# Performance work log

Hardware: AMD Instinct MI355X
Metric: run time of the kernel (lower is better)

## Reference

```python
import jax, jax.numpy as jnp
import numpy as np

H = 64
EPS = 1e-5


def _lstm_layer(x, w_ih, w_hh, b_ih, b_hh):
    """Single LSTM layer, batch_first input x: [B, T, I]. PyTorch gate order i,f,g,o."""
    B, T, _ = x.shape
    # precompute input contributions for all timesteps: [B, T, 4H]
    xw = jnp.einsum('bti,gi->btg', x, w_ih) + (b_ih + b_hh)
    xw = jnp.swapaxes(xw, 0, 1)  # [T, B, 4H] for scan over time

    def step(carry, xw_t):
        h, c = carry
        gates = xw_t + h @ w_hh.T  # [B, 4H]
        i, f, g, o = jnp.split(gates, 4, axis=-1)
        i = jax.nn.sigmoid(i)
        f = jax.nn.sigmoid(f)
        g = jnp.tanh(g)
        o = jax.nn.sigmoid(o)
        c = f * c + i * g
        h = o * jnp.tanh(c)
        return (h, c), h

    h0 = jnp.zeros((B, H), x.dtype)
    (_, _), hs = jax.lax.scan(step, (h0, h0), xw)
    return jnp.swapaxes(hs, 0, 1)  # [B, T, H]


def setup_inputs() -> dict:
    key = jax.random.key(0)
    ks = jax.random.split(key, 16)
    B, T, F = 4096, 256, 32
    s = 1.0 / np.sqrt(H)  # PyTorch LSTM init scale
    inp = {
        'x': jax.random.normal(ks[0], (B, T, F), jnp.float32),
        'w_ih0': jax.random.uniform(ks[1], (4 * H, F), jnp.float32, -s, s),
        'w_hh0': jax.random.uniform(ks[2], (4 * H, H), jnp.float32, -s, s),
        'b_ih0': jax.random.uniform(ks[3], (4 * H,), jnp.float32, -s, s),
        'b_hh0': jax.random.uniform(ks[4], (4 * H,), jnp.float32, -s, s),
        'w_ih1': jax.random.uniform(ks[5], (4 * H, H), jnp.float32, -s, s),
        'w_hh1': jax.random.uniform(ks[6], (4 * H, H), jnp.float32, -s, s),
        'b_ih1': jax.random.uniform(ks[7], (4 * H,), jnp.float32, -s, s),
        'b_hh1': jax.random.uniform(ks[8], (4 * H,), jnp.float32, -s, s),
        'ln_g': jnp.ones((H,), jnp.float32),
        'ln_b': jnp.zeros((H,), jnp.float32),
        'w1': jax.random.uniform(ks[9], (64, H), jnp.float32, -s, s),
        'b1': jax.random.uniform(ks[10], (64,), jnp.float32, -s, s),
        'w2': jax.random.uniform(ks[11], (1, 64), jnp.float32, -0.125, 0.125),
        'b2': jax.random.uniform(ks[12], (1,), jnp.float32, -0.125, 0.125),
    }
    return inp


def reference(x, w_ih0, w_hh0, b_ih0, b_hh0, w_ih1, w_hh1, b_ih1, b_hh1,
              ln_g, ln_b, w1, b1, w2, b2):
    out0 = _lstm_layer(x, w_ih0, w_hh0, b_ih0, b_hh0)      # [B, T, H]
    out1 = _lstm_layer(out0, w_ih1, w_hh1, b_ih1, b_hh1)   # [B, T, H]
    last = out1[:, -1, :]                                   # [B, H]
    # LayerNorm
    mu = jnp.mean(last, axis=-1, keepdims=True)
    var = jnp.mean(jnp.square(last - mu), axis=-1, keepdims=True)
    ln = (last - mu) * jax.lax.rsqrt(var + EPS) * ln_g + ln_b
    # MLP head
    h = jax.nn.relu(ln @ w1.T + b1)
    y = h @ w2.T + b2                                       # [B, 1]
    return y[:, 0]
```

## Files before the change

kernel.cpp:

```cpp
#include <hip/hip_runtime.h>

#define TSEQ 256
#define FIN  32
#define HID  64

typedef _Float16 f16x8 __attribute__((ext_vector_type(8)));
typedef float    f32x4 __attribute__((ext_vector_type(4)));

__device__ __forceinline__ float wsum(float v) {
    #pragma unroll
    for (int off = 32; off > 0; off >>= 1) v += __shfl_xor(v, off, 64);
    return v;
}

__device__ __forceinline__ float lstm_cell(const f32x4 g, float& c) {
    float ei = __expf(-g[0]);
    float ef = __expf(-g[1]);
    float yg = __expf(2.0f * g[2]);
    float eo = __expf(-g[3]);
    float sf = __builtin_amdgcn_rcpf(1.0f + ef);
    float ig = (yg - 1.0f) * __builtin_amdgcn_rcpf((1.0f + ei) * (yg + 1.0f));
    c = fmaf(sf, c, ig);
    float cc = fminf(fmaxf(c, -15.0f), 15.0f);
    float yc = __expf(2.0f * cc);
    return (yc - 1.0f) * __builtin_amdgcn_rcpf((1.0f + eo) * (yc + 1.0f));
}

__global__ __launch_bounds__(1024, 4)
void lstm_fused(const float* __restrict__ x,
                const float* __restrict__ w_ih0, const float* __restrict__ w_hh0,
                const float* __restrict__ b_ih0, const float* __restrict__ b_hh0,
                const float* __restrict__ w_ih1, const float* __restrict__ w_hh1,
                const float* __restrict__ b_ih1, const float* __restrict__ b_hh1,
                const float* __restrict__ ln_g, const float* __restrict__ ln_b,
                const float* __restrict__ w1, const float* __restrict__ b1,
                const float* __restrict__ w2, const float* __restrict__ b2,
                float* __restrict__ out)
{
    __shared__ __align__(16) _Float16 X[2][16][32];
    __shared__ __align__(16) _Float16 H0[2][16][72];
    __shared__ __align__(16) _Float16 H1[2][16][72];
    __shared__ __align__(16) float HF[16][68];
    __shared__ __align__(16) float LNB[16][64];

    const int tid  = threadIdx.x;
    const int wave = tid >> 6;
    const int lane = tid & 63;
    const int q    = lane >> 4;
    const int lm   = lane & 15;
    const int q8   = q * 8;
    const int b0   = blockIdx.x * 16;

    const int np   = wave * 16 + lm;
    const int drow = np >> 2;
    const int ty   = np & 3;
    const int row  = ty * 64 + drow;
    const int dq   = wave * 4 + q;

    f16x8 w0f[3], w1f[4];
    f32x4 bias0, bias1;
    {
        const float* p0 = w_ih0 + row * FIN + q8;
        const float* p1 = w_hh0 + row * HID + q8;
        const float* p2 = w_hh0 + row * HID + 32 + q8;
        const float* p3 = w_ih1 + row * HID + q8;
        const float* p4 = w_ih1 + row * HID + 32 + q8;
        const float* p5 = w_hh1 + row * HID + q8;
        const float* p6 = w_hh1 + row * HID + 32 + q8;
        #pragma unroll
        for (int j = 0; j < 8; ++j) {
            w0f[0][j] = (_Float16)p0[j];
            w0f[1][j] = (_Float16)p1[j];
            w0f[2][j] = (_Float16)p2[j];
            w1f[0][j] = (_Float16)p3[j];
            w1f[1][j] = (_Float16)p4[j];
            w1f[2][j] = (_Float16)p5[j];
            w1f[3][j] = (_Float16)p6[j];
        }
        #pragma unroll
        for (int r = 0; r < 4; ++r) {
            bias0[r] = b_ih0[r * 64 + dq] + b_hh0[r * 64 + dq];
            bias1[r] = b_ih1[r * 64 + dq] + b_hh1[r * 64 + dq];
        }
    }

    for (int i = tid; i < 2 * 16 * 72; i += 1024) {
        ((_Float16*)H0)[i] = (_Float16)0.0f;
        ((_Float16*)H1)[i] = (_Float16)0.0f;
    }
    const bool xlane = lane < 32;
    const int  xcol  = lane & 31;
    const float* xbase = x + (size_t)(b0 + wave) * TSEQ * FIN + xcol;
    if (xlane) X[0][wave][xcol] = (_Float16)xbase[0];
    float xw = xbase[FIN];

    float c0 = 0.0f, c1 = 0.0f;
    __syncthreads();

#define INTERVAL(P, DO_A, DO_B, DO_XSTORE, DO_XLOAD, XI)                        \
    {                                                                           \
        float xnew = 0.0f;                                                      \
        if (DO_XLOAD) xnew = xbase[(size_t)(XI) * FIN];                         \
        f16x8 rh0a = *reinterpret_cast<const f16x8*>(&H0[(P) ^ 1][lm][q8]);     \
        f16x8 rh0b = *reinterpret_cast<const f16x8*>(&H0[(P) ^ 1][lm][32 + q8]);\
        if (DO_A) {                                                             \
            f16x8 rx = *reinterpret_cast<const f16x8*>(&X[P][lm][q8]);          \
            f32x4 aA = bias0;                                                   \
            aA = __builtin_amdgcn_mfma_f32_16x16x32_f16(w0f[0], rx,   aA, 0, 0, 0); \
            aA = __builtin_amdgcn_mfma_f32_16x16x32_f16(w0f[1], rh0a, aA, 0, 0, 0); \
            aA = __builtin_amdgcn_mfma_f32_16x16x32_f16(w0f[2], rh0b, aA, 0, 0, 0); \
            float hA = lstm_cell(aA, c0);                                       \
            H0[P][lm][dq] = (_Float16)hA;                                       \
        }                                                                       \
        if (DO_B) {                                                             \
            f16x8 rh1a = *reinterpret_cast<const f16x8*>(&H1[P][lm][q8]);       \
            f16x8 rh1b = *reinterpret_cast<const f16x8*>(&H1[P][lm][32 + q8]);  \
            f32x4 aB = bias1;                                                   \
            aB = __builtin_amdgcn_mfma_f32_16x16x32_f16(w1f[0], rh0a, aB, 0, 0, 0); \
            aB = __builtin_amdgcn_mfma_f32_16x16x32_f16(w1f[1], rh0b, aB, 0, 0, 0); \
            aB = __builtin_amdgcn_mfma_f32_16x16x32_f16(w1f[2], rh1a, aB, 0, 0, 0); \
            aB = __builtin_amdgcn_mfma_f32_16x16x32_f16(w1f[3], rh1b, aB, 0, 0, 0); \
            float hB = lstm_cell(aB, c1);                                       \
            H1[(P) ^ 1][lm][dq] = (_Float16)hB;                                 \
            lastB = hB;                                                         \
        }                                                                       \
        if (DO_XSTORE && xlane) X[(P) ^ 1][wave][xcol] = (_Float16)xw;          \
        xw = xnew;                                                              \
        __syncthreads();                                                        \
    }

    float lastB = 0.0f;

    INTERVAL(0, true, false, true, true, 2)

    #pragma unroll 1
    for (int ii = 0; ii < 127; ++ii) {
        const int i1  = 2 * ii + 1;
        const int xiA = (i1 + 2 > 255) ? 255 : i1 + 2;
        const int xiB = (i1 + 3 > 255) ? 255 : i1 + 3;
        INTERVAL(1, true, true, true, true, xiA)
        INTERVAL(0, true, true, true, true, xiB)
    }

    INTERVAL(1, true, true, false, false, 0)
    INTERVAL(0, false, true, false, false, 0)
    HF[lm][dq] = lastB;
    __syncthreads();

#undef INTERVAL

    const float lngv = ln_g[lane], lnbv = ln_b[lane];
    const float b1v = b1[lane], w2v = w2[lane];
    const float* w1row = w1 + lane * 64;
    {
        float v  = HF[wave][lane];
        float mu = wsum(v) * (1.0f / 64.0f);
        float dv = v - mu;
        float var = wsum(dv * dv) * (1.0f / 64.0f);
        float ln = dv * rsqrtf(var + 1e-5f) * lngv + lnbv;
        LNB[wave][lane] = ln;
        float s = b1v;
        #pragma unroll
        for (int dd = 0; dd < 64; ++dd)
            s = fmaf(LNB[wave][dd], w1row[dd], s);
        s = fmaxf(s, 0.0f);
        float y = wsum(s * w2v);
        if (lane == 0) out[b0 + wave] = y + b2[0];
    }
}

extern "C" void kernel_launch(void* const* d_in, const int* in_sizes, int n_in,
                              void* d_out, int out_size, void* d_ws, size_t ws_size,
                              hipStream_t stream) {
    const float* x     = (const float*)d_in[0];
    const float* w_ih0 = (const float*)d_in[1];
    const float* w_hh0 = (const float*)d_in[2];
    const float* b_ih0 = (const float*)d_in[3];
    const float* b_hh0 = (const float*)d_in[4];
    const float* w_ih1 = (const float*)d_in[5];
    const float* w_hh1 = (const float*)d_in[6];
    const float* b_ih1 = (const float*)d_in[7];
    const float* b_hh1 = (const float*)d_in[8];
    const float* ln_g  = (const float*)d_in[9];
    const float* ln_b  = (const float*)d_in[10];
    const float* w1    = (const float*)d_in[11];
    const float* b1    = (const float*)d_in[12];
    const float* w2    = (const float*)d_in[13];
    const float* b2    = (const float*)d_in[14];
    lstm_fused<<<dim3(256), dim3(1024), 0, stream>>>(
        x, w_ih0, w_hh0, b_ih0, b_hh0,
        w_ih1, w_hh1, b_ih1, b_hh1,
        ln_g, ln_b, w1, b1, w2, b2, (float*)d_out);
}
```

Measured before the change: 370.5 us.

## Halve batch per block and split gate tiles across two MFMA sets per wave

Each block now handles 8 sequences with 8 waves instead of 16 sequences with 16 waves. Each wave keeps two gate-tile weight sets and issues two interleaved MFMA chains per layer. The 16-column MFMA is half-used, with the upper 8 columns padded by zeroed X. The two accumulators are merged into one lane-packed f32x4 via a DPP row-rotate, so each lane still runs one LSTM cell. This doubles the number of blocks and gives more independent MFMA work per wave, in exchange for wasted MFMA columns, doubled weight registers and extra DPP/select ops.

Result: slower. 439.3 us (+18.6%).

```diff
diff --git a/kernel.cpp b/kernel.cpp
--- a/kernel.cpp
+++ b/kernel.cpp
@@ -11,6 +11,11 @@
     #pragma unroll
     for (int off = 32; off > 0; off >>= 1) v += __shfl_xor(v, off, 64);
     return v;
+}
+
+__device__ __forceinline__ float ror8(float v) {
+    return __int_as_float(__builtin_amdgcn_update_dpp(
+        0, __float_as_int(v), 0x128, 0xF, 0xF, true));
 }
 
 __device__ __forceinline__ float lstm_cell(const f32x4 g, float& c) {
@@ -26,7 +31,7 @@
     return (yc - 1.0f) * __builtin_amdgcn_rcpf((1.0f + eo) * (yc + 1.0f));
 }
 
-__global__ __launch_bounds__(1024, 4)
+__global__ __launch_bounds__(512, 4)
 void lstm_fused(const float* __restrict__ x,
                 const float* __restrict__ w_ih0, const float* __restrict__ w_hh0,
                 const float* __restrict__ b_ih0, const float* __restrict__ b_hh0,
@@ -40,8 +45,8 @@
     __shared__ __align__(16) _Float16 X[2][16][32];
     __shared__ __align__(16) _Float16 H0[2][16][72];
     __shared__ __align__(16) _Float16 H1[2][16][72];
-    __shared__ __align__(16) float HF[16][68];
-    __shared__ __align__(16) float LNB[16][64];
+    __shared__ __align__(16) float HF[8][68];
+    __shared__ __align__(16) float LNB[8][64];
 
     const int tid  = threadIdx.x;
     const int wave = tid >> 6;
@@ -49,17 +54,23 @@
     const int q    = lane >> 4;
     const int lm   = lane & 15;
     const int q8   = q * 8;
-    const int b0   = blockIdx.x * 16;
-
-    const int np   = wave * 16 + lm;
-    const int drow = np >> 2;
-    const int ty   = np & 3;
-    const int row  = ty * 64 + drow;
-    const int dq   = wave * 4 + q;
-
-    f16x8 w0f[3], w1f[4];
-    f32x4 bias0, bias1;
-    {
+    const int b0   = blockIdx.x * 8;
+
+    const int blm = lm & 7;
+    const int pd  = (lm < 8) ? (wave * 4 + q) : ((wave + 8) * 4 + q);
+
+    f16x8 w0fA[3], w0fB[3], w1fA[4], w1fB[4];
+    f32x4 bias0A, bias0B, bias1A, bias1B;
+    #pragma unroll
+    for (int tb = 0; tb < 2; ++tb) {
+        const int T    = wave + 8 * tb;
+        const int np   = T * 16 + lm;
+        const int drow = np >> 2;
+        const int ty   = np & 3;
+        const int row  = ty * 64 + drow;
+        const int dq   = T * 4 + q;
+        f16x8* w0f = tb ? w0fB : w0fA;
+        f16x8* w1f = tb ? w1fB : w1fA;
         const float* p0 = w_ih0 + row * FIN + q8;
         const float* p1 = w_hh0 + row * HID + q8;
         const float* p2 = w_hh0 + row * HID + 32 + q8;
@@ -77,17 +88,22 @@
             w1f[2][j] = (_Float16)p5[j];
             w1f[3][j] = (_Float16)p6[j];
         }
+        f32x4 bb0, bb1;
         #pragma unroll
         for (int r = 0; r < 4; ++r) {
-            bias0[r] = b_ih0[r * 64 + dq] + b_hh0[r * 64 + dq];
-            bias1[r] = b_ih1[r * 64 + dq] + b_hh1[r * 64 + dq];
+            bb0[r] = b_ih0[r * 64 + dq] + b_hh0[r * 64 + dq];
+            bb1[r] = b_ih1[r * 64 + dq] + b_hh1[r * 64 + dq];
         }
-    }
-
-    for (int i = tid; i < 2 * 16 * 72; i += 1024) {
+        if (tb) { bias0B = bb0; bias1B = bb1; } else { bias0A = bb0; bias1A = bb1; }
+    }
+
+    for (int i = tid; i < 2 * 16 * 72; i += 512) {
         ((_Float16*)H0)[i] = (_Float16)0.0f;
         ((_Float16*)H1)[i] = (_Float16)0.0f;
     }
+    for (int i = tid; i < 2 * 16 * 32; i += 512) ((_Float16*)X)[i] = (_Float16)0.0f;
+    __syncthreads();
+
     const bool xlane = lane < 32;
     const int  xcol  = lane & 31;
     const float* xbase = x + (size_t)(b0 + wave) * TSEQ * FIN + xcol;
@@ -96,6 +112,15 @@
 
     float c0 = 0.0f, c1 = 0.0f;
     __syncthreads();
+
+#define PACK(dst, a0v, a1v)                                                     \
+    {                                                                           \
+        _Pragma("unroll")                                                       \
+        for (int r = 0; r < 4; ++r) {                                           \
+            float rv = ror8(a1v[r]);                                            \
+            dst[r] = (lm < 8) ? a0v[r] : rv;                                    \
+        }                                                                       \
+    }
 
 #define INTERVAL(P, DO_A, DO_B, DO_XSTORE, DO_XLOAD, XI)                        \
     {                                                                           \
@@ -105,23 +130,32 @@
         f16x8 rh0b = *reinterpret_cast<const f16x8*>(&H0[(P) ^ 1][lm][32 + q8]);\
         if (DO_A) {                                                             \
             f16x8 rx = *reinterpret_cast<const f16x8*>(&X[P][lm][q8]);          \
-            f32x4 aA = bias0;                                                   \
-            aA = __builtin_amdgcn_mfma_f32_16x16x32_f16(w0f[0], rx,   aA, 0, 0, 0); \
-            aA = __builtin_amdgcn_mfma_f32_16x16x32_f16(w0f[1], rh0a, aA, 0, 0, 0); \
-            aA = __builtin_amdgcn_mfma_f32_16x16x32_f16(w0f[2], rh0b, aA, 0, 0, 0); \
-            float hA = lstm_cell(aA, c0);                                       \
-            H0[P][lm][dq] = (_Float16)hA;                                       \
+            f32x4 a0 = bias0A, a1 = bias0B;                                     \
+            a0 = __builtin_amdgcn_mfma_f32_16x16x32_f16(w0fA[0], rx,   a0, 0, 0, 0); \
+            a1 = __builtin_amdgcn_mfma_f32_16x16x32_f16(w0fB[0], rx,   a1, 0, 0, 0); \
+            a0 = __builtin_amdgcn_mfma_f32_16x16x32_f16(w0fA[1], rh0a, a0, 0, 0, 0); \
+            a1 = __builtin_amdgcn_mfma_f32_16x16x32_f16(w0fB[1], rh0a, a1, 0, 0, 0); \
+            a0 = __builtin_amdgcn_mfma_f32_16x16x32_f16(w0fA[2], rh0b, a0, 0, 0, 0); \
+            a1 = __builtin_amdgcn_mfma_f32_16x16x32_f16(w0fB[2], rh0b, a1, 0, 0, 0); \
+            f32x4 pa; PACK(pa, a0, a1)                                          \
+            float hA = lstm_cell(pa, c0);                                       \
+            H0[P][blm][pd] = (_Float16)hA;                                      \
         }                                                                       \
         if (DO_B) {                                                             \
             f16x8 rh1a = *reinterpret_cast<const f16x8*>(&H1[P][lm][q8]);       \
             f16x8 rh1b = *reinterpret_cast<const f16x8*>(&H1[P][lm][32 + q8]);  \
-            f32x4 aB = bias1;                                                   \
-            aB = __builtin_amdgcn_mfma_f32_16x16x32_f16(w1f[0], rh0a, aB, 0, 0, 0); \
-            aB = __builtin_amdgcn_mfma_f32_16x16x32_f16(w1f[1], rh0b, aB, 0, 0, 0); \
-            aB = __builtin_amdgcn_mfma_f32_16x16x32_f16(w1f[2], rh1a, aB, 0, 0, 0); \
-            aB = __builtin_amdgcn_mfma_f32_16x16x32_f16(w1f[3], rh1b, aB, 0, 0, 0); \
-            float hB = lstm_cell(aB, c1);                                       \
-            H1[(P) ^ 1][lm][dq] = (_Float16)hB;                                 \
+            f32x4 a0 = bias1A, a1 = bias1B;                                     \
+            a0 = __builtin_amdgcn_mfma_f32_16x16x32_f16(w1fA[0], rh0a, a0, 0, 0, 0); \
+            a1 = __builtin_amdgcn_mfma_f32_16x16x32_f16(w1fB[0], rh0a, a1, 0, 0, 0); \
+            a0 = __builtin_amdgcn_mfma_f32_16x16x32_f16(w1fA[1], rh0b, a0, 0, 0, 0); \
+            a1 = __builtin_amdgcn_mfma_f32_16x16x32_f16(w1fB[1], rh0b, a1, 0, 0, 0); \
+            a0 = __builtin_amdgcn_mfma_f32_16x16x32_f16(w1fA[2], rh1a, a0, 0, 0, 0); \
+            a1 = __builtin_amdgcn_mfma_f32_16x16x32_f16(w1fB[2], rh1a, a1, 0, 0, 0); \
+            a0 = __builtin_amdgcn_mfma_f32_16x16x32_f16(w1fA[3], rh1b, a0, 0, 0, 0); \
+            a1 = __builtin_amdgcn_mfma_f32_16x16x32_f16(w1fB[3], rh1b, a1, 0, 0, 0); \
+            f32x4 pb; PACK(pb, a0, a1)                                          \
+            float hB = lstm_cell(pb, c1);                                       \
+            H1[(P) ^ 1][blm][pd] = (_Float16)hB;                                \
             lastB = hB;                                                         \
         }                                                                       \
         if (DO_XSTORE && xlane) X[(P) ^ 1][wave][xcol] = (_Float16)xw;          \
@@ -144,10 +178,11 @@
 
     INTERVAL(1, true, true, false, false, 0)
     INTERVAL(0, false, true, false, false, 0)
-    HF[lm][dq] = lastB;
+    HF[blm][pd] = lastB;
     __syncthreads();
 
 #undef INTERVAL
+#undef PACK
 
     const float lngv = ln_g[lane], lnbv = ln_b[lane];
     const float b1v = b1[lane], w2v = w2[lane];
@@ -187,7 +222,7 @@
     const float* b1    = (const float*)d_in[12];
     const float* w2    = (const float*)d_in[13];
     const float* b2    = (const float*)d_in[14];
-    lstm_fused<<<dim3(256), dim3(1024), 0, stream>>>(
+    lstm_fused<<<dim3(512), dim3(512), 0, stream>>>(
         x, w_ih0, w_hh0, b_ih0, b_hh0,
         w_ih1, w_hh1, b_ih1, b_hh1,
         ln_g, ln_b, w1, b1, w2, b2, (float*)d_out);
```
